# Optimization experiments

Measured on AMD Instinct MI355X. Metric: run time of the kernel, lower is better.

Reference implementation:

```python
import jax, jax.numpy as jnp
import numpy as np

NUM_LAYERS = 2
NUM_RES_LAYERS = 1  # residual add applied to layers i >= NUM_LAYERS - NUM_RES_LAYERS


def _lstm_seq(x, W, U, b, reverse):
    """Keras-style LSTM over full sequence. x:[B,T,E], W:[E,4H], U:[H,4H], b:[4H].
    Gate order i,f,g,o (Keras). reverse=True emulates go_backwards + K.reverse
    (lax.scan reverse=True keeps outputs time-aligned). Returns [B,T,H]."""
    B = x.shape[0]
    H = U.shape[0]
    # precompute input projections for all timesteps in one big matmul
    zx = jnp.einsum('bte,eg->btg', x, W) + b  # [B,T,4H]
    zx = jnp.swapaxes(zx, 0, 1)  # [T,B,4H]

    def step(carry, zxt):
        h, c = carry
        z = zxt + h @ U  # [B,4H]
        i, f, g, o = jnp.split(z, 4, axis=-1)
        i = jax.nn.sigmoid(i)
        f = jax.nn.sigmoid(f)
        g = jnp.tanh(g)
        o = jax.nn.sigmoid(o)
        c = f * c + i * g
        h = o * jnp.tanh(c)
        return (h, c), h

    init = (jnp.zeros((B, H), x.dtype), jnp.zeros((B, H), x.dtype))
    _, hs = jax.lax.scan(step, init, zx, reverse=reverse)  # [T,B,H]
    return jnp.swapaxes(hs, 0, 1)


def setup_inputs() -> dict:
    key = jax.random.key(0)
    k1, k2, k3 = jax.random.split(key, 3)
    B, T, E, H = 512, 200, 128, 128
    s = 0.05  # keep gates in a sane regime
    x = jax.random.normal(k1, (B, T, E), dtype=jnp.float32)
    W = jax.random.normal(k2, (NUM_LAYERS, 2, E, 4 * H), dtype=jnp.float32) * s
    U = jax.random.normal(k3, (NUM_LAYERS, 2, H, 4 * H), dtype=jnp.float32) * s
    b = jnp.ones((NUM_LAYERS, 2, 4 * H), dtype=jnp.float32)  # bias_initializer='ones'
    return {"x": x, "W": W, "U": U, "b": b}


def reference(x, W, U, b):
    # inference mode: dropout inactive
    input_fw = x
    input_bw = x
    for i in range(NUM_LAYERS):
        out_fw = _lstm_seq(input_fw, W[i, 0], U[i, 0], b[i, 0], reverse=False)
        out_bw = _lstm_seq(input_bw, W[i, 1], U[i, 1], b[i, 1], reverse=True)
        if i >= NUM_LAYERS - NUM_RES_LAYERS:
            out_fw = out_fw + input_fw
            out_bw = out_bw + input_bw
        input_fw = out_fw
        input_bw = out_bw
    # mode == 'ave'
    return (input_fw + input_bw) / 2
```

## Files before the change

kernel.cpp:

```cpp
#include <hip/hip_runtime.h>


typedef _Float16 f16;
typedef _Float16 f16x2 __attribute__((ext_vector_type(2)));
typedef _Float16 f16x4 __attribute__((ext_vector_type(4)));
typedef _Float16 f16x8 __attribute__((ext_vector_type(8)));
typedef float    f32x4 __attribute__((ext_vector_type(4)));

#define B_   512
#define T_   200
#define E_   128
#define H_   128
#define G4_  512
#define M_   (B_*T_)

static __device__ __forceinline__ float rcpa(float x) {
#if __has_builtin(__builtin_amdgcn_rcpf)
  return __builtin_amdgcn_rcpf(x);
#else
  return 1.f / x;
#endif
}
static __device__ __forceinline__ float exp2a(float x) {
#if __has_builtin(__builtin_amdgcn_exp2f)
  return __builtin_amdgcn_exp2f(x);
#else
  return exp2f(x);
#endif
}
static __device__ __forceinline__ f16x2 pk2(float lo, float hi) {
  return __builtin_bit_cast(f16x2, __builtin_amdgcn_cvt_pkrtz(lo, hi));
}

static __device__ __forceinline__ void lgkm_barrier() {
  asm volatile("s_waitcnt lgkmcnt(0)" ::: "memory");
  __builtin_amdgcn_s_barrier();
}

__global__ __launch_bounds__(256)
void cvt_x(const float* __restrict__ x, f16* __restrict__ xh) {
  const int n8 = M_ * E_ / 8;
  for (int i = blockIdx.x * 256 + threadIdx.x; i < n8; i += gridDim.x * 256) {
    const float4 a = ((const float4*)x)[i * 2];
    const float4 b = ((const float4*)x)[i * 2 + 1];
    f16x8 v;
    v[0] = (f16)a.x; v[1] = (f16)a.y; v[2] = (f16)a.z; v[3] = (f16)a.w;
    v[4] = (f16)b.x; v[5] = (f16)b.y; v[6] = (f16)b.z; v[7] = (f16)b.w;
    *(f16x8*)(xh + (size_t)i * 8) = v;
  }
}

__global__ __launch_bounds__(256)
void prep_w(const float* __restrict__ W, const float* __restrict__ U,
            f16* __restrict__ Wt, f16* __restrict__ Ut) {
  const int m = blockIdx.x;
  const float* s = (m < 4 ? W + (size_t)m * E_ * G4_ : U + (size_t)(m - 4) * E_ * G4_);
  f16* d        = (m < 4 ? Wt + (size_t)m * E_ * G4_ : Ut + (size_t)(m - 4) * E_ * G4_);
  for (int i = threadIdx.x; i < E_ * G4_; i += 256) {
    const int k = i >> 9, g = i & 511;
    float v = s[i];
    if ((g >> 7) == 2) v *= 2.f;
    d[(size_t)g * E_ + k] = (f16)v;
  }
}

template <int LAYER>
__global__ __launch_bounds__(512, 2)
void scan_fused(const f16* __restrict__ in,
                const f16* __restrict__ Utl,
                const f16* __restrict__ Wtl,
                const float* __restrict__ bl,
                const f16* __restrict__ res,
                f16* __restrict__ hout)
{
  __shared__ f16 hsh[2][16][136];

  const int tid  = threadIdx.x;
  const int lane = tid & 63;
  const int wv   = tid >> 6;
  const int row  = lane & 15;
  const int kg   = lane >> 4;
  const int bx   = blockIdx.x;
  const int dir  = bx >> 5;
  const int R0   = (bx & 31) * 16;
  const int coff = wv * 16 + kg * 4;

  const f16* Ud = Utl + (size_t)dir * G4_ * E_;
  const f16* Wd = Wtl + (size_t)dir * G4_ * E_;
  const float* bd = bl + (size_t)dir * G4_;
  const f16* ind  = in + (LAYER == 1 ? (size_t)dir * M_ * H_ : 0);
  f16* houtd      = hout + (size_t)dir * M_ * H_;

  f16x8 aU[4][4], aW[4][4];
#pragma unroll
  for (int g = 0; g < 4; ++g) {
    const size_t gcol = (size_t)(g * 128 + wv * 16 + row) * E_;
#pragma unroll
    for (int kk = 0; kk < 4; ++kk) {
      aU[g][kk] = *(const f16x8*)(Ud + gcol + kk * 32 + kg * 8);
      aW[g][kk] = *(const f16x8*)(Wd + gcol + kk * 32 + kg * 8);
    }
  }
  f32x4 zb[4];
#pragma unroll
  for (int g = 0; g < 4; ++g) {
#pragma unroll
    for (int i = 0; i < 4; ++i) {
      const float v = bd[g * 128 + coff + i];
      zb[g][i] = (g == 2) ? 2.f * v : v;
    }
  }

  for (int i = tid; i < 2 * 16 * 136; i += 512) ((f16*)hsh)[i] = (f16)0.f;

  const int t0 = dir ? (T_ - 1) : 0;
  const int ts = dir ? -1 : 1;

  const f16* inrow  = ind + (size_t)(R0 + row) * T_ * E_ + kg * 8;
  const f16* resrow = (LAYER == 1)
      ? res + (size_t)dir * M_ * H_ + (size_t)(R0 + row) * T_ * H_ + coff : nullptr;
  f16* outptr = houtd + (size_t)(R0 + row) * T_ * H_ + (size_t)t0 * H_ + coff;

  float cc0 = 0.f, cc1 = 0.f, cc2 = 0.f, cc3 = 0.f;

  const f16* xptrA = inrow + (long)(t0 + ts) * E_;
  const f16* xptrB = inrow + (long)(t0 + 2 * ts) * E_;
  f16x8 xpA[4], xpB[4], xP[4];
#pragma unroll
  for (int kk = 0; kk < 4; ++kk) {
    xP[kk]  = *(const f16x8*)(inrow + (long)t0 * E_ + kk * 32);
    xpA[kk] = *(const f16x8*)(xptrA + kk * 32);
    xpB[kk] = *(const f16x8*)(xptrB + kk * 32);
  }
  const f16* rptrA = nullptr; const f16* rptrB = nullptr;
  uint2 rvA = {}, rvB = {};
  if (LAYER == 1) {
    rptrA = resrow + (long)t0 * H_;
    rptrB = resrow + (long)(t0 + ts) * H_;
    rvA = *(const uint2*)rptrA;
    rvB = *(const uint2*)rptrB;
  }

  lgkm_barrier();

  f32x4 zA[4], zB[4];
#pragma unroll
  for (int g = 0; g < 4; ++g) {
    zA[g] = __builtin_amdgcn_mfma_f32_16x16x32_f16(aW[g][0], xP[0], zb[g], 0, 0, 0);
#pragma unroll
    for (int kk = 1; kk < 4; ++kk)
      zA[g] = __builtin_amdgcn_mfma_f32_16x16x32_f16(aW[g][kk], xP[kk], zA[g], 0, 0, 0);
  }

  constexpr float NL2E  = -1.4426950408889634f;
  constexpr float NL2E2 = -2.8853900817779268f;

  auto step = [&](f32x4 (&zc)[4], f32x4 (&zn)[4], f16x8 (&xp)[4],
                  const f16*& xptr, uint2& rv, const f16*& rptr,
                  int rp, int wp) {
    f16x8 hf[4];
#pragma unroll
    for (int kk = 0; kk < 4; ++kk) hf[kk] = *(const f16x8*)&hsh[rp][row][kk * 32 + kg * 8];

#pragma unroll
    for (int g = 0; g < 4; ++g)
      zn[g] = __builtin_amdgcn_mfma_f32_16x16x32_f16(aW[g][0], xp[0], zb[g], 0, 0, 0);
#pragma unroll
    for (int kk = 1; kk < 4; ++kk) {
      zn[0] = __builtin_amdgcn_mfma_f32_16x16x32_f16(aW[0][kk], xp[kk], zn[0], 0, 0, 0);
      zn[1] = __builtin_amdgcn_mfma_f32_16x16x32_f16(aW[1][kk], xp[kk], zn[1], 0, 0, 0);
      zn[2] = __builtin_amdgcn_mfma_f32_16x16x32_f16(aW[2][kk], xp[kk], zn[2], 0, 0, 0);
      zn[3] = __builtin_amdgcn_mfma_f32_16x16x32_f16(aW[3][kk], xp[kk], zn[3], 0, 0, 0);
    }

    xptr += 2 * ts * E_;
#pragma unroll
    for (int kk = 0; kk < 4; ++kk) xp[kk] = *(const f16x8*)(xptr + kk * 32);
    f16x2 rva, rvb;
    if (LAYER == 1) {
      rva = __builtin_bit_cast(f16x2, rv.x);
      rvb = __builtin_bit_cast(f16x2, rv.y);
      rptr += 2 * ts * H_;
      rv = *(const uint2*)rptr;
    }

#pragma unroll
    for (int kk = 0; kk < 4; ++kk) {
      zc[0] = __builtin_amdgcn_mfma_f32_16x16x32_f16(aU[0][kk], hf[kk], zc[0], 0, 0, 0);
      zc[1] = __builtin_amdgcn_mfma_f32_16x16x32_f16(aU[1][kk], hf[kk], zc[1], 0, 0, 0);
      zc[2] = __builtin_amdgcn_mfma_f32_16x16x32_f16(aU[2][kk], hf[kk], zc[2], 0, 0, 0);
      zc[3] = __builtin_amdgcn_mfma_f32_16x16x32_f16(aU[3][kk], hf[kk], zc[3], 0, 0, 0);
    }

    float hv[4];
    float cc[4] = {cc0, cc1, cc2, cc3};
#pragma unroll
    for (int i = 0; i < 4; ++i) {
      const float ei = exp2a(zc[0][i] * NL2E);
      const float ef = exp2a(zc[1][i] * NL2E);
      const float eg = exp2a(zc[2][i] * NL2E);
      const float eo = exp2a(zc[3][i] * NL2E);
      const float ig = rcpa(1.f + ei);
      const float fg = rcpa(1.f + ef);
      const float gg = fmaf(2.f, rcpa(1.f + eg), -1.f);
      const float og = rcpa(1.f + eo);
      cc[i] = fmaf(fg, cc[i], ig * gg);
      const float ec = exp2a(cc[i] * NL2E2);
      const float tc = fmaf(2.f, rcpa(1.f + ec), -1.f);
      hv[i] = og * tc;
    }
    cc0 = cc[0]; cc1 = cc[1]; cc2 = cc[2]; cc3 = cc[3];

    const f16x2 h01 = pk2(hv[0], hv[1]);
    const f16x2 h23 = pk2(hv[2], hv[3]);
    uint2 hp;
    hp.x = __builtin_bit_cast(unsigned int, h01);
    hp.y = __builtin_bit_cast(unsigned int, h23);
    *(uint2*)&hsh[wp][row][coff] = hp;

    if (LAYER == 0) {
      *(uint2*)outptr = hp;
    } else {
      const f16x2 half2 = {(f16)0.5f, (f16)0.5f};
      const f16x2 o01 = (h01 + rva) * half2;
      const f16x2 o23 = (h23 + rvb) * half2;
      uint2 o;
      o.x = __builtin_bit_cast(unsigned int, o01);
      o.y = __builtin_bit_cast(unsigned int, o23);
      *(uint2*)outptr = o;
    }
    outptr += ts * H_;

    lgkm_barrier();
  };

  for (int k = 0; k < T_ / 2; ++k) {
    step(zA, zB, xpA, xptrA, rvA, rptrA, 0, 1);
    step(zB, zA, xpB, xptrB, rvB, rptrB, 1, 0);
  }
}

__global__ __launch_bounds__(256)
void final_add(const f16* __restrict__ a, const f16* __restrict__ b,
               float* __restrict__ o)
{
  const int n8 = M_ * H_ / 8;
  for (int i = blockIdx.x * 256 + threadIdx.x; i < n8; i += gridDim.x * 256) {
    const f16x8 va = *(const f16x8*)(a + (size_t)i * 8);
    const f16x8 vb = *(const f16x8*)(b + (size_t)i * 8);
    float4 o0, o1;
    o0.x = (float)va[0] + (float)vb[0];  o0.y = (float)va[1] + (float)vb[1];
    o0.z = (float)va[2] + (float)vb[2];  o0.w = (float)va[3] + (float)vb[3];
    o1.x = (float)va[4] + (float)vb[4];  o1.y = (float)va[5] + (float)vb[5];
    o1.z = (float)va[6] + (float)vb[6];  o1.w = (float)va[7] + (float)vb[7];
    *(float4*)(o + (size_t)i * 8)     = o0;
    *(float4*)(o + (size_t)i * 8 + 4) = o1;
  }
}

extern "C" void kernel_launch(void* const* d_in, const int* in_sizes, int n_in,
                              void* d_out, int out_size, void* d_ws, size_t ws_size,
                              hipStream_t stream) {
  const float* x = (const float*)d_in[0];
  const float* W = (const float*)d_in[1];
  const float* U = (const float*)d_in[2];
  const float* b = (const float*)d_in[3];
  float* out = (float*)d_out;

  char* ws = (char*)d_ws;
  f16* xh = (f16*)(ws + 2048);
  f16* h0 = xh + (size_t)M_ * E_ + 1024;
  f16* h1 = h0 + (size_t)2 * M_ * H_ + 1024;
  f16* Wt = h1 + (size_t)2 * M_ * H_ + 1024;
  f16* Ut = Wt + (size_t)4 * G4_ * E_;

  const size_t WTL = (size_t)2 * G4_ * E_;
  const size_t BL  = 2 * G4_;

  cvt_x<<<dim3(2048), 256, 0, stream>>>(x, xh);
  prep_w<<<dim3(8), 256, 0, stream>>>(W, U, Wt, Ut);
  scan_fused<0><<<dim3(64), 512, 0, stream>>>(xh, Ut, Wt, b, nullptr, h0);
  scan_fused<1><<<dim3(64), 512, 0, stream>>>(h0, Ut + WTL, Wt + WTL, b + BL, h0, h1);
  final_add<<<dim3(2048), 256, 0, stream>>>(h1, h1 + (size_t)M_ * H_, out);
}
```

Baseline: 636.1 us.

## Interleave input-projection MFMAs with gate math and fold log2e into weights

The -log2(e) scale factor is folded into the W and U weights and into the bias at prep time, which removes the per-gate multiply before exp2. The next step's input-projection MFMAs are spread through the gate-activation loop so matrix work overlaps the transcendental ALU work. The barrier now sits right after the shared-memory h write, and the global output store plus the next x and residual loads come after it, so they overlap the next step. Scaling the weights before the f16 conversion slightly changes rounding.

Measured after the change: 728.7 us. 14.5% more time.

```diff
diff --git a/kernel.cpp b/kernel.cpp
--- a/kernel.cpp
+++ b/kernel.cpp
@@ -56,11 +56,11 @@
   const int m = blockIdx.x;
   const float* s = (m < 4 ? W + (size_t)m * E_ * G4_ : U + (size_t)(m - 4) * E_ * G4_);
   f16* d        = (m < 4 ? Wt + (size_t)m * E_ * G4_ : Ut + (size_t)(m - 4) * E_ * G4_);
+  const float L2E = 1.4426950408889634f;
   for (int i = threadIdx.x; i < E_ * G4_; i += 256) {
     const int k = i >> 9, g = i & 511;
-    float v = s[i];
-    if ((g >> 7) == 2) v *= 2.f;
-    d[(size_t)g * E_ + k] = (f16)v;
+    const float sc = ((g >> 7) == 2) ? -2.f * L2E : -L2E;
+    d[(size_t)g * E_ + k] = (f16)(s[i] * sc);
   }
 }
 
@@ -101,13 +101,14 @@
       aW[g][kk] = *(const f16x8*)(Wd + gcol + kk * 32 + kg * 8);
     }
   }
+  const float L2E = 1.4426950408889634f;
   f32x4 zb[4];
 #pragma unroll
   for (int g = 0; g < 4; ++g) {
 #pragma unroll
     for (int i = 0; i < 4; ++i) {
       const float v = bd[g * 128 + coff + i];
-      zb[g][i] = (g == 2) ? 2.f * v : v;
+      zb[g][i] = v * ((g == 2) ? -2.f * L2E : -L2E);
     }
   }
 
@@ -152,7 +153,6 @@
       zA[g] = __builtin_amdgcn_mfma_f32_16x16x32_f16(aW[g][kk], xP[kk], zA[g], 0, 0, 0);
   }
 
-  constexpr float NL2E  = -1.4426950408889634f;
   constexpr float NL2E2 = -2.8853900817779268f;
 
   auto step = [&](f32x4 (&zc)[4], f32x4 (&zn)[4], f16x8 (&xp)[4],
@@ -161,28 +161,6 @@
     f16x8 hf[4];
 #pragma unroll
     for (int kk = 0; kk < 4; ++kk) hf[kk] = *(const f16x8*)&hsh[rp][row][kk * 32 + kg * 8];
-
-#pragma unroll
-    for (int g = 0; g < 4; ++g)
-      zn[g] = __builtin_amdgcn_mfma_f32_16x16x32_f16(aW[g][0], xp[0], zb[g], 0, 0, 0);
-#pragma unroll
-    for (int kk = 1; kk < 4; ++kk) {
-      zn[0] = __builtin_amdgcn_mfma_f32_16x16x32_f16(aW[0][kk], xp[kk], zn[0], 0, 0, 0);
-      zn[1] = __builtin_amdgcn_mfma_f32_16x16x32_f16(aW[1][kk], xp[kk], zn[1], 0, 0, 0);
-      zn[2] = __builtin_amdgcn_mfma_f32_16x16x32_f16(aW[2][kk], xp[kk], zn[2], 0, 0, 0);
-      zn[3] = __builtin_amdgcn_mfma_f32_16x16x32_f16(aW[3][kk], xp[kk], zn[3], 0, 0, 0);
-    }
-
-    xptr += 2 * ts * E_;
-#pragma unroll
-    for (int kk = 0; kk < 4; ++kk) xp[kk] = *(const f16x8*)(xptr + kk * 32);
-    f16x2 rva, rvb;
-    if (LAYER == 1) {
-      rva = __builtin_bit_cast(f16x2, rv.x);
-      rvb = __builtin_bit_cast(f16x2, rv.y);
-      rptr += 2 * ts * H_;
-      rv = *(const uint2*)rptr;
-    }
 
 #pragma unroll
     for (int kk = 0; kk < 4; ++kk) {
@@ -196,10 +174,21 @@
     float cc[4] = {cc0, cc1, cc2, cc3};
 #pragma unroll
     for (int i = 0; i < 4; ++i) {
-      const float ei = exp2a(zc[0][i] * NL2E);
-      const float ef = exp2a(zc[1][i] * NL2E);
-      const float eg = exp2a(zc[2][i] * NL2E);
-      const float eo = exp2a(zc[3][i] * NL2E);
+      if (i == 0) {
+        zn[0] = __builtin_amdgcn_mfma_f32_16x16x32_f16(aW[0][0], xp[0], zb[0], 0, 0, 0);
+        zn[1] = __builtin_amdgcn_mfma_f32_16x16x32_f16(aW[1][0], xp[0], zb[1], 0, 0, 0);
+        zn[2] = __builtin_amdgcn_mfma_f32_16x16x32_f16(aW[2][0], xp[0], zb[2], 0, 0, 0);
+        zn[3] = __builtin_amdgcn_mfma_f32_16x16x32_f16(aW[3][0], xp[0], zb[3], 0, 0, 0);
+      } else {
+        zn[0] = __builtin_amdgcn_mfma_f32_16x16x32_f16(aW[0][i], xp[i], zn[0], 0, 0, 0);
+        zn[1] = __builtin_amdgcn_mfma_f32_16x16x32_f16(aW[1][i], xp[i], zn[1], 0, 0, 0);
+        zn[2] = __builtin_amdgcn_mfma_f32_16x16x32_f16(aW[2][i], xp[i], zn[2], 0, 0, 0);
+        zn[3] = __builtin_amdgcn_mfma_f32_16x16x32_f16(aW[3][i], xp[i], zn[3], 0, 0, 0);
+      }
+      const float ei = exp2a(zc[0][i]);
+      const float ef = exp2a(zc[1][i]);
+      const float eg = exp2a(zc[2][i]);
+      const float eo = exp2a(zc[3][i]);
       const float ig = rcpa(1.f + ei);
       const float fg = rcpa(1.f + ef);
       const float gg = fmaf(2.f, rcpa(1.f + eg), -1.f);
@@ -218,20 +207,27 @@
     hp.y = __builtin_bit_cast(unsigned int, h23);
     *(uint2*)&hsh[wp][row][coff] = hp;
 
+    lgkm_barrier();
+
     if (LAYER == 0) {
       *(uint2*)outptr = hp;
     } else {
       const f16x2 half2 = {(f16)0.5f, (f16)0.5f};
+      const f16x2 rva = __builtin_bit_cast(f16x2, rv.x);
+      const f16x2 rvb = __builtin_bit_cast(f16x2, rv.y);
       const f16x2 o01 = (h01 + rva) * half2;
       const f16x2 o23 = (h23 + rvb) * half2;
       uint2 o;
       o.x = __builtin_bit_cast(unsigned int, o01);
       o.y = __builtin_bit_cast(unsigned int, o23);
       *(uint2*)outptr = o;
+      rptr += 2 * ts * H_;
+      rv = *(const uint2*)rptr;
     }
     outptr += ts * H_;
-
-    lgkm_barrier();
+    xptr += 2 * ts * E_;
+#pragma unroll
+    for (int kk = 0; kk < 4; ++kk) xp[kk] = *(const f16x8*)(xptr + kk * 32);
   };
 
   for (int k = 0; k < T_ / 2; ++k) {
```

## Hoist input projection out of LSTM scan into a separate parallel GEMM

Applied to the files above, without the earlier changes.

The input-projection matmul (x·W + b) for every timestep now runs in a standalone tiled MFMA GEMM over the whole grid, for both directions. The result is stored as an f16 z buffer, with the -log2(e) and gate-specific scale already folded into W and b. The recurrent scan kernel then only does the h·U MFMAs and the gate math each step, prefetching the precomputed z two steps ahead. U is loaded from fp32 and transposed through shared memory inside the scan, which drops the separate weight and x conversion kernels. The aim is to shorten the per-step serial critical path on only 64 blocks. The cost is writing and re-reading a large z intermediate in memory, plus extra precision loss from storing pre-activations in f16.

Measured after the change: 795.0 us. 1.25x slower.

```diff
diff --git a/kernel.cpp b/kernel.cpp
--- a/kernel.cpp
+++ b/kernel.cpp
@@ -14,6 +14,9 @@
 #define G4_  512
 #define M_   (B_*T_)
 
+constexpr float NL2E  = -1.4426950408889634f;
+constexpr float NL2E2 = -2.8853900817779268f;
+
 static __device__ __forceinline__ float rcpa(float x) {
 #if __has_builtin(__builtin_amdgcn_rcpf)
   return __builtin_amdgcn_rcpf(x);
@@ -31,48 +34,105 @@
 static __device__ __forceinline__ f16x2 pk2(float lo, float hi) {
   return __builtin_bit_cast(f16x2, __builtin_amdgcn_cvt_pkrtz(lo, hi));
 }
-
 static __device__ __forceinline__ void lgkm_barrier() {
   asm volatile("s_waitcnt lgkmcnt(0)" ::: "memory");
   __builtin_amdgcn_s_barrier();
 }
 
+template <typename AT>
 __global__ __launch_bounds__(256)
-void cvt_x(const float* __restrict__ x, f16* __restrict__ xh) {
-  const int n8 = M_ * E_ / 8;
-  for (int i = blockIdx.x * 256 + threadIdx.x; i < n8; i += gridDim.x * 256) {
-    const float4 a = ((const float4*)x)[i * 2];
-    const float4 b = ((const float4*)x)[i * 2 + 1];
-    f16x8 v;
-    v[0] = (f16)a.x; v[1] = (f16)a.y; v[2] = (f16)a.z; v[3] = (f16)a.w;
-    v[4] = (f16)b.x; v[5] = (f16)b.y; v[6] = (f16)b.z; v[7] = (f16)b.w;
-    *(f16x8*)(xh + (size_t)i * 8) = v;
-  }
-}
-
-__global__ __launch_bounds__(256)
-void prep_w(const float* __restrict__ W, const float* __restrict__ U,
-            f16* __restrict__ Wt, f16* __restrict__ Ut) {
-  const int m = blockIdx.x;
-  const float* s = (m < 4 ? W + (size_t)m * E_ * G4_ : U + (size_t)(m - 4) * E_ * G4_);
-  f16* d        = (m < 4 ? Wt + (size_t)m * E_ * G4_ : Ut + (size_t)(m - 4) * E_ * G4_);
-  for (int i = threadIdx.x; i < E_ * G4_; i += 256) {
-    const int k = i >> 9, g = i & 511;
-    float v = s[i];
-    if ((g >> 7) == 2) v *= 2.f;
-    d[(size_t)g * E_ + k] = (f16)v;
+void gemm_zx(const AT* __restrict__ A0, const AT* __restrict__ A1,
+             const float* __restrict__ Wl,
+             const float* __restrict__ bl,
+             f16* __restrict__ zx)
+{
+  __shared__ f16 Ash[128 * 136];
+  __shared__ f16 Bsh[64 * 136];
+
+  const int n0  = blockIdx.x * 64;
+  const int m0  = blockIdx.y * 128;
+  const int dir = blockIdx.z;
+  const AT* A = dir ? A1 : A0;
+  const float* Wd = Wl + (size_t)dir * E_ * G4_;
+  const float* bd = bl + (size_t)dir * G4_;
+  const int tid = threadIdx.x;
+
+#pragma unroll
+  for (int it = 0; it < 16; ++it) {
+    int idx = tid + it * 256;
+    int row = idx >> 5, c4 = idx & 31;
+    if constexpr (sizeof(AT) == 4) {
+      const float4 v = *(const float4*)(A + (size_t)(m0 + row) * E_ + c4 * 4);
+      f16x2 p0; p0[0] = (f16)v.x; p0[1] = (f16)v.y;
+      f16x2 p1; p1[0] = (f16)v.z; p1[1] = (f16)v.w;
+      uint2 w2; w2.x = __builtin_bit_cast(unsigned int, p0); w2.y = __builtin_bit_cast(unsigned int, p1);
+      *(uint2*)&Ash[row * 136 + c4 * 4] = w2;
+    } else {
+      const uint2 v = *(const uint2*)(A + (size_t)(m0 + row) * E_ + c4 * 4);
+      *(uint2*)&Ash[row * 136 + c4 * 4] = v;
+    }
+  }
+#pragma unroll
+  for (int it = 0; it < 8; ++it) {
+    int idx = tid + it * 256;
+    int k = idx >> 4, n4 = idx & 15;
+    const int g = n0 + n4 * 4;
+    const float sc = ((g >> 7) == 2) ? NL2E2 : NL2E;
+    const float4 v = *(const float4*)(Wd + (size_t)k * G4_ + g);
+    Bsh[(n4 * 4 + 0) * 136 + k] = (f16)(v.x * sc);
+    Bsh[(n4 * 4 + 1) * 136 + k] = (f16)(v.y * sc);
+    Bsh[(n4 * 4 + 2) * 136 + k] = (f16)(v.z * sc);
+    Bsh[(n4 * 4 + 3) * 136 + k] = (f16)(v.w * sc);
+  }
+  __syncthreads();
+
+  const int w = tid >> 6, l = tid & 63;
+  const int lr = l & 15, lk = (l >> 4) * 8;
+  f32x4 acc[2][4] = {};
+
+#pragma unroll
+  for (int kc = 0; kc < 4; ++kc) {
+    const int kb = kc * 32 + lk;
+    f16x8 a0 = *(const f16x8*)&Ash[(w * 32 + 0  + lr) * 136 + kb];
+    f16x8 a1 = *(const f16x8*)&Ash[(w * 32 + 16 + lr) * 136 + kb];
+    f16x8 b0 = *(const f16x8*)&Bsh[(0  + lr) * 136 + kb];
+    f16x8 b1 = *(const f16x8*)&Bsh[(16 + lr) * 136 + kb];
+    f16x8 b2 = *(const f16x8*)&Bsh[(32 + lr) * 136 + kb];
+    f16x8 b3 = *(const f16x8*)&Bsh[(48 + lr) * 136 + kb];
+    acc[0][0] = __builtin_amdgcn_mfma_f32_16x16x32_f16(a0, b0, acc[0][0], 0, 0, 0);
+    acc[0][1] = __builtin_amdgcn_mfma_f32_16x16x32_f16(a0, b1, acc[0][1], 0, 0, 0);
+    acc[0][2] = __builtin_amdgcn_mfma_f32_16x16x32_f16(a0, b2, acc[0][2], 0, 0, 0);
+    acc[0][3] = __builtin_amdgcn_mfma_f32_16x16x32_f16(a0, b3, acc[0][3], 0, 0, 0);
+    acc[1][0] = __builtin_amdgcn_mfma_f32_16x16x32_f16(a1, b0, acc[1][0], 0, 0, 0);
+    acc[1][1] = __builtin_amdgcn_mfma_f32_16x16x32_f16(a1, b1, acc[1][1], 0, 0, 0);
+    acc[1][2] = __builtin_amdgcn_mfma_f32_16x16x32_f16(a1, b2, acc[1][2], 0, 0, 0);
+    acc[1][3] = __builtin_amdgcn_mfma_f32_16x16x32_f16(a1, b3, acc[1][3], 0, 0, 0);
+  }
+
+#pragma unroll
+  for (int mf = 0; mf < 2; ++mf) {
+#pragma unroll
+    for (int nf = 0; nf < 4; ++nf) {
+      const int g = n0 + nf * 16 + lr;
+      const float sc = ((g >> 7) == 2) ? NL2E2 : NL2E;
+      const float bias = bd[g] * sc;
+#pragma unroll
+      for (int i = 0; i < 4; ++i) {
+        const int m = m0 + w * 32 + mf * 16 + (l >> 4) * 4 + i;
+        zx[((size_t)dir * M_ + m) * G4_ + g] = (f16)(acc[mf][nf][i] + bias);
+      }
+    }
   }
 }
 
 template <int LAYER>
 __global__ __launch_bounds__(512, 2)
-void scan_fused(const f16* __restrict__ in,
-                const f16* __restrict__ Utl,
-                const f16* __restrict__ Wtl,
-                const float* __restrict__ bl,
-                const f16* __restrict__ res,
-                f16* __restrict__ hout)
+void scan_u(const f16* __restrict__ zx,
+            const float* __restrict__ Ul,
+            const f16* __restrict__ res,
+            f16* __restrict__ hout)
 {
+  __shared__ f16 Ush[32][520];
   __shared__ f16 hsh[2][16][136];
 
   const int tid  = threadIdx.x;
@@ -85,30 +145,35 @@
   const int R0   = (bx & 31) * 16;
   const int coff = wv * 16 + kg * 4;
 
-  const f16* Ud = Utl + (size_t)dir * G4_ * E_;
-  const f16* Wd = Wtl + (size_t)dir * G4_ * E_;
-  const float* bd = bl + (size_t)dir * G4_;
-  const f16* ind  = in + (LAYER == 1 ? (size_t)dir * M_ * H_ : 0);
-  f16* houtd      = hout + (size_t)dir * M_ * H_;
-
-  f16x8 aU[4][4], aW[4][4];
-#pragma unroll
-  for (int g = 0; g < 4; ++g) {
-    const size_t gcol = (size_t)(g * 128 + wv * 16 + row) * E_;
-#pragma unroll
-    for (int kk = 0; kk < 4; ++kk) {
-      aU[g][kk] = *(const f16x8*)(Ud + gcol + kk * 32 + kg * 8);
-      aW[g][kk] = *(const f16x8*)(Wd + gcol + kk * 32 + kg * 8);
-    }
-  }
-  f32x4 zb[4];
-#pragma unroll
-  for (int g = 0; g < 4; ++g) {
-#pragma unroll
-    for (int i = 0; i < 4; ++i) {
-      const float v = bd[g * 128 + coff + i];
-      zb[g][i] = (g == 2) ? 2.f * v : v;
-    }
+  const float* Udr = Ul + (size_t)dir * H_ * G4_;
+  const f16* zxd   = zx + (size_t)dir * M_ * G4_;
+  f16* houtd       = hout + (size_t)dir * M_ * H_;
+
+  f16x8 aU[4][4];
+#pragma unroll
+  for (int c = 0; c < 4; ++c) {
+#pragma unroll
+    for (int it = 0; it < 8; ++it) {
+      const int idx = tid + it * 512;
+      const int kl = idx >> 7, g4 = idx & 127;
+      const float4 v = *(const float4*)(Udr + (size_t)(c * 32 + kl) * G4_ + g4 * 4);
+      const int g = g4 * 4;
+      const float sc = ((g >> 7) == 2) ? NL2E2 : NL2E;
+      Ush[kl][g + 0] = (f16)(v.x * sc);
+      Ush[kl][g + 1] = (f16)(v.y * sc);
+      Ush[kl][g + 2] = (f16)(v.z * sc);
+      Ush[kl][g + 3] = (f16)(v.w * sc);
+    }
+    __syncthreads();
+#pragma unroll
+    for (int g = 0; g < 4; ++g) {
+      const int gcol = g * 128 + wv * 16 + row;
+      f16x8 t;
+#pragma unroll
+      for (int j = 0; j < 8; ++j) t[j] = Ush[kg * 8 + j][gcol];
+      aU[g][c] = t;
+    }
+    __syncthreads();
   }
 
   for (int i = tid; i < 2 * 16 * 136; i += 512) ((f16*)hsh)[i] = (f16)0.f;
@@ -116,90 +181,72 @@
   const int t0 = dir ? (T_ - 1) : 0;
   const int ts = dir ? -1 : 1;
 
-  const f16* inrow  = ind + (size_t)(R0 + row) * T_ * E_ + kg * 8;
-  const f16* resrow = (LAYER == 1)
-      ? res + (size_t)dir * M_ * H_ + (size_t)(R0 + row) * T_ * H_ + coff : nullptr;
-  f16* outptr = houtd + (size_t)(R0 + row) * T_ * H_ + (size_t)t0 * H_ + coff;
-
-  float cc0 = 0.f, cc1 = 0.f, cc2 = 0.f, cc3 = 0.f;
-
-  const f16* xptrA = inrow + (long)(t0 + ts) * E_;
-  const f16* xptrB = inrow + (long)(t0 + 2 * ts) * E_;
-  f16x8 xpA[4], xpB[4], xP[4];
-#pragma unroll
-  for (int kk = 0; kk < 4; ++kk) {
-    xP[kk]  = *(const f16x8*)(inrow + (long)t0 * E_ + kk * 32);
-    xpA[kk] = *(const f16x8*)(xptrA + kk * 32);
-    xpB[kk] = *(const f16x8*)(xptrB + kk * 32);
+  const f16* zrow = zxd + ((size_t)(R0 + row) * T_ + t0) * G4_ + coff;
+  const f16* zptrA = zrow;
+  const f16* zptrB = zrow + (long)ts * G4_;
+  f16x4 zpA[4], zpB[4];
+#pragma unroll
+  for (int g = 0; g < 4; ++g) {
+    zpA[g] = *(const f16x4*)(zptrA + g * 128);
+    zpB[g] = *(const f16x4*)(zptrB + g * 128);
   }
   const f16* rptrA = nullptr; const f16* rptrB = nullptr;
   uint2 rvA = {}, rvB = {};
   if (LAYER == 1) {
+    const f16* resrow = res + (size_t)dir * M_ * H_ + (size_t)(R0 + row) * T_ * H_ + coff;
     rptrA = resrow + (long)t0 * H_;
     rptrB = resrow + (long)(t0 + ts) * H_;
     rvA = *(const uint2*)rptrA;
     rvB = *(const uint2*)rptrB;
   }
+  f16* outptr = houtd + (size_t)(R0 + row) * T_ * H_ + (size_t)t0 * H_ + coff;
+
+  float cc0 = 0.f, cc1 = 0.f, cc2 = 0.f, cc3 = 0.f;
 
   lgkm_barrier();
 
-  f32x4 zA[4], zB[4];
-#pragma unroll
-  for (int g = 0; g < 4; ++g) {
-    zA[g] = __builtin_amdgcn_mfma_f32_16x16x32_f16(aW[g][0], xP[0], zb[g], 0, 0, 0);
-#pragma unroll
-    for (int kk = 1; kk < 4; ++kk)
-      zA[g] = __builtin_amdgcn_mfma_f32_16x16x32_f16(aW[g][kk], xP[kk], zA[g], 0, 0, 0);
-  }
-
-  constexpr float NL2E  = -1.4426950408889634f;
-  constexpr float NL2E2 = -2.8853900817779268f;
-
-  auto step = [&](f32x4 (&zc)[4], f32x4 (&zn)[4], f16x8 (&xp)[4],
-                  const f16*& xptr, uint2& rv, const f16*& rptr,
+  auto step = [&](f16x4 (&zp)[4], const f16*& zptr, uint2& rv, const f16*& rptr,
                   int rp, int wp) {
     f16x8 hf[4];
 #pragma unroll
     for (int kk = 0; kk < 4; ++kk) hf[kk] = *(const f16x8*)&hsh[rp][row][kk * 32 + kg * 8];
 
-#pragma unroll
-    for (int g = 0; g < 4; ++g)
-      zn[g] = __builtin_amdgcn_mfma_f32_16x16x32_f16(aW[g][0], xp[0], zb[g], 0, 0, 0);
-#pragma unroll
-    for (int kk = 1; kk < 4; ++kk) {
-      zn[0] = __builtin_amdgcn_mfma_f32_16x16x32_f16(aW[0][kk], xp[kk], zn[0], 0, 0, 0);
-      zn[1] = __builtin_amdgcn_mfma_f32_16x16x32_f16(aW[1][kk], xp[kk], zn[1], 0, 0, 0);
-      zn[2] = __builtin_amdgcn_mfma_f32_16x16x32_f16(aW[2][kk], xp[kk], zn[2], 0, 0, 0);
-      zn[3] = __builtin_amdgcn_mfma_f32_16x16x32_f16(aW[3][kk], xp[kk], zn[3], 0, 0, 0);
-    }
-
-    xptr += 2 * ts * E_;
-#pragma unroll
-    for (int kk = 0; kk < 4; ++kk) xp[kk] = *(const f16x8*)(xptr + kk * 32);
+    f32x4 z[4];
+#pragma unroll
+    for (int g = 0; g < 4; ++g) {
+#pragma unroll
+      for (int i = 0; i < 4; ++i) z[g][i] = (float)zp[g][i];
+    }
     f16x2 rva, rvb;
     if (LAYER == 1) {
       rva = __builtin_bit_cast(f16x2, rv.x);
       rvb = __builtin_bit_cast(f16x2, rv.y);
+    }
+
+    zptr += 2 * ts * G4_;
+#pragma unroll
+    for (int g = 0; g < 4; ++g) zp[g] = *(const f16x4*)(zptr + g * 128);
+    if (LAYER == 1) {
       rptr += 2 * ts * H_;
       rv = *(const uint2*)rptr;
     }
 
 #pragma unroll
     for (int kk = 0; kk < 4; ++kk) {
-      zc[0] = __builtin_amdgcn_mfma_f32_16x16x32_f16(aU[0][kk], hf[kk], zc[0], 0, 0, 0);
-      zc[1] = __builtin_amdgcn_mfma_f32_16x16x32_f16(aU[1][kk], hf[kk], zc[1], 0, 0, 0);
-      zc[2] = __builtin_amdgcn_mfma_f32_16x16x32_f16(aU[2][kk], hf[kk], zc[2], 0, 0, 0);
-      zc[3] = __builtin_amdgcn_mfma_f32_16x16x32_f16(aU[3][kk], hf[kk], zc[3], 0, 0, 0);
+      z[0] = __builtin_amdgcn_mfma_f32_16x16x32_f16(aU[0][kk], hf[kk], z[0], 0, 0, 0);
+      z[1] = __builtin_amdgcn_mfma_f32_16x16x32_f16(aU[1][kk], hf[kk], z[1], 0, 0, 0);
+      z[2] = __builtin_amdgcn_mfma_f32_16x16x32_f16(aU[2][kk], hf[kk], z[2], 0, 0, 0);
+      z[3] = __builtin_amdgcn_mfma_f32_16x16x32_f16(aU[3][kk], hf[kk], z[3], 0, 0, 0);
     }
 
     float hv[4];
     float cc[4] = {cc0, cc1, cc2, cc3};
 #pragma unroll
     for (int i = 0; i < 4; ++i) {
-      const float ei = exp2a(zc[0][i] * NL2E);
-      const float ef = exp2a(zc[1][i] * NL2E);
-      const float eg = exp2a(zc[2][i] * NL2E);
-      const float eo = exp2a(zc[3][i] * NL2E);
+      const float ei = exp2a(z[0][i]);
+      const float ef = exp2a(z[1][i]);
+      const float eg = exp2a(z[2][i]);
+      const float eo = exp2a(z[3][i]);
       const float ig = rcpa(1.f + ei);
       const float fg = rcpa(1.f + ef);
       const float gg = fmaf(2.f, rcpa(1.f + eg), -1.f);
@@ -235,8 +282,8 @@
   };
 
   for (int k = 0; k < T_ / 2; ++k) {
-    step(zA, zB, xpA, xptrA, rvA, rptrA, 0, 1);
-    step(zB, zA, xpB, xptrB, rvB, rptrB, 1, 0);
+    step(zpA, zptrA, rvA, rptrA, 0, 1);
+    step(zpB, zptrB, rvB, rptrB, 1, 0);
   }
 }
 
@@ -268,18 +315,16 @@
   float* out = (float*)d_out;
 
   char* ws = (char*)d_ws;
-  f16* xh = (f16*)(ws + 2048);
-  f16* h0 = xh + (size_t)M_ * E_ + 1024;
-  f16* h1 = h0 + (size_t)2 * M_ * H_ + 1024;
-  f16* Wt = h1 + (size_t)2 * M_ * H_ + 1024;
-  f16* Ut = Wt + (size_t)4 * G4_ * E_;
-
-  const size_t WTL = (size_t)2 * G4_ * E_;
-  const size_t BL  = 2 * G4_;
-
-  cvt_x<<<dim3(2048), 256, 0, stream>>>(x, xh);
-  prep_w<<<dim3(8), 256, 0, stream>>>(W, U, Wt, Ut);
-  scan_fused<0><<<dim3(64), 512, 0, stream>>>(xh, Ut, Wt, b, nullptr, h0);
-  scan_fused<1><<<dim3(64), 512, 0, stream>>>(h0, Ut + WTL, Wt + WTL, b + BL, h0, h1);
-  final_add<<<dim3(2048), 256, 0, stream>>>(h1, h1 + (size_t)M_ * H_, out);
-}
+  f16* zx = (f16*)ws;
+  f16* h0 = (f16*)(ws + (size_t)2 * M_ * G4_ * 2);
+
+  const size_t WL = (size_t)2 * E_ * G4_;
+  const size_t BL = 2 * G4_;
+
+  dim3 gg(G4_ / 64, M_ / 128, 2);
+  gemm_zx<float><<<gg, 256, 0, stream>>>(x, x, W, b, zx);
+  scan_u<0><<<dim3(64), 512, 0, stream>>>(zx, U, nullptr, h0);
+  gemm_zx<f16><<<gg, 256, 0, stream>>>(h0, h0 + (size_t)M_ * H_, W + WL, b + BL, zx);
+  scan_u<1><<<dim3(64), 512, 0, stream>>>(zx, U + WL, h0, h0);
+  final_add<<<dim3(2048), 256, 0, stream>>>(h0, h0 + (size_t)M_ * H_, out);
+}
```

## Halve waves per scan block, give each wave two column tiles, fold log2e scale into weights

Applied to the files above, without the earlier changes.

The recurrent scan kernel now runs 4 waves of 256 threads instead of 8. Each wave computes two 16-column tiles, so it holds twice the W/U fragments in registers. This cuts barrier participants and the per-step synchronisation cost, but puts more serial MFMA work on each wave and raises register pressure. The -log2(e) and -2·log2(e) gate scaling is folded into the f16 weights and bias in prep, removing per-element multiplies, at some f16 precision risk. The cross-step software pipelining of the input projection is also dropped, so x-projection MFMAs are now issued in the same step as the recurrent ones.

Result: slower. 709.3 us (+11.5%).

```diff
diff --git a/kernel.cpp b/kernel.cpp
--- a/kernel.cpp
+++ b/kernel.cpp
@@ -14,6 +14,9 @@
 #define G4_  512
 #define M_   (B_*T_)
 
+constexpr float NL2E  = -1.4426950408889634f;
+constexpr float NL2E2 = -2.8853900817779268f;
+
 static __device__ __forceinline__ float rcpa(float x) {
 #if __has_builtin(__builtin_amdgcn_rcpf)
   return __builtin_amdgcn_rcpf(x);
@@ -31,7 +34,6 @@
 static __device__ __forceinline__ f16x2 pk2(float lo, float hi) {
   return __builtin_bit_cast(f16x2, __builtin_amdgcn_cvt_pkrtz(lo, hi));
 }
-
 static __device__ __forceinline__ void lgkm_barrier() {
   asm volatile("s_waitcnt lgkmcnt(0)" ::: "memory");
   __builtin_amdgcn_s_barrier();
@@ -58,14 +60,13 @@
   f16* d        = (m < 4 ? Wt + (size_t)m * E_ * G4_ : Ut + (size_t)(m - 4) * E_ * G4_);
   for (int i = threadIdx.x; i < E_ * G4_; i += 256) {
     const int k = i >> 9, g = i & 511;
-    float v = s[i];
-    if ((g >> 7) == 2) v *= 2.f;
-    d[(size_t)g * E_ + k] = (f16)v;
+    const float sc = ((g >> 7) == 2) ? NL2E2 : NL2E;
+    d[(size_t)g * E_ + k] = (f16)(s[i] * sc);
   }
 }
 
 template <int LAYER>
-__global__ __launch_bounds__(512, 2)
+__global__ __launch_bounds__(256, 1)
 void scan_fused(const f16* __restrict__ in,
                 const f16* __restrict__ Utl,
                 const f16* __restrict__ Wtl,
@@ -83,7 +84,7 @@
   const int bx   = blockIdx.x;
   const int dir  = bx >> 5;
   const int R0   = (bx & 31) * 16;
-  const int coff = wv * 16 + kg * 4;
+  const int c0   = wv * 32 + kg * 4;
 
   const f16* Ud = Utl + (size_t)dir * G4_ * E_;
   const f16* Wd = Wtl + (size_t)dir * G4_ * E_;
@@ -91,143 +92,157 @@
   const f16* ind  = in + (LAYER == 1 ? (size_t)dir * M_ * H_ : 0);
   f16* houtd      = hout + (size_t)dir * M_ * H_;
 
-  f16x8 aU[4][4], aW[4][4];
+  f16x8 aU[4][2][4], aW[4][2][4];
 #pragma unroll
   for (int g = 0; g < 4; ++g) {
-    const size_t gcol = (size_t)(g * 128 + wv * 16 + row) * E_;
-#pragma unroll
-    for (int kk = 0; kk < 4; ++kk) {
-      aU[g][kk] = *(const f16x8*)(Ud + gcol + kk * 32 + kg * 8);
-      aW[g][kk] = *(const f16x8*)(Wd + gcol + kk * 32 + kg * 8);
-    }
-  }
-  f32x4 zb[4];
+#pragma unroll
+    for (int ct = 0; ct < 2; ++ct) {
+      const size_t gcol = (size_t)(g * 128 + wv * 32 + ct * 16 + row) * E_;
+#pragma unroll
+      for (int kk = 0; kk < 4; ++kk) {
+        aU[g][ct][kk] = *(const f16x8*)(Ud + gcol + kk * 32 + kg * 8);
+        aW[g][ct][kk] = *(const f16x8*)(Wd + gcol + kk * 32 + kg * 8);
+      }
+    }
+  }
+  f32x4 zb[4][2];
 #pragma unroll
   for (int g = 0; g < 4; ++g) {
 #pragma unroll
-    for (int i = 0; i < 4; ++i) {
-      const float v = bd[g * 128 + coff + i];
-      zb[g][i] = (g == 2) ? 2.f * v : v;
-    }
-  }
-
-  for (int i = tid; i < 2 * 16 * 136; i += 512) ((f16*)hsh)[i] = (f16)0.f;
+    for (int ct = 0; ct < 2; ++ct) {
+#pragma unroll
+      for (int i = 0; i < 4; ++i) {
+        const float v = bd[g * 128 + wv * 32 + ct * 16 + kg * 4 + i];
+        zb[g][ct][i] = v * ((g == 2) ? NL2E2 : NL2E);
+      }
+    }
+  }
+
+  for (int i = tid; i < 2 * 16 * 136; i += 256) ((f16*)hsh)[i] = (f16)0.f;
 
   const int t0 = dir ? (T_ - 1) : 0;
   const int ts = dir ? -1 : 1;
 
   const f16* inrow  = ind + (size_t)(R0 + row) * T_ * E_ + kg * 8;
   const f16* resrow = (LAYER == 1)
-      ? res + (size_t)dir * M_ * H_ + (size_t)(R0 + row) * T_ * H_ + coff : nullptr;
-  f16* outptr = houtd + (size_t)(R0 + row) * T_ * H_ + (size_t)t0 * H_ + coff;
-
-  float cc0 = 0.f, cc1 = 0.f, cc2 = 0.f, cc3 = 0.f;
-
-  const f16* xptrA = inrow + (long)(t0 + ts) * E_;
-  const f16* xptrB = inrow + (long)(t0 + 2 * ts) * E_;
-  f16x8 xpA[4], xpB[4], xP[4];
+      ? res + (size_t)dir * M_ * H_ + (size_t)(R0 + row) * T_ * H_ + c0 : nullptr;
+  f16* outptr = houtd + (size_t)(R0 + row) * T_ * H_ + (size_t)t0 * H_ + c0;
+
+  float cc[8] = {0.f, 0.f, 0.f, 0.f, 0.f, 0.f, 0.f, 0.f};
+
+  const f16* xptrA = inrow + (long)t0 * E_;
+  const f16* xptrB = inrow + (long)(t0 + ts) * E_;
+  f16x8 xpA[4], xpB[4];
 #pragma unroll
   for (int kk = 0; kk < 4; ++kk) {
-    xP[kk]  = *(const f16x8*)(inrow + (long)t0 * E_ + kk * 32);
     xpA[kk] = *(const f16x8*)(xptrA + kk * 32);
     xpB[kk] = *(const f16x8*)(xptrB + kk * 32);
   }
   const f16* rptrA = nullptr; const f16* rptrB = nullptr;
-  uint2 rvA = {}, rvB = {};
+  uint2 rvA[2] = {}, rvB[2] = {};
   if (LAYER == 1) {
     rptrA = resrow + (long)t0 * H_;
     rptrB = resrow + (long)(t0 + ts) * H_;
-    rvA = *(const uint2*)rptrA;
-    rvB = *(const uint2*)rptrB;
+    rvA[0] = *(const uint2*)rptrA;      rvA[1] = *(const uint2*)(rptrA + 16);
+    rvB[0] = *(const uint2*)rptrB;      rvB[1] = *(const uint2*)(rptrB + 16);
   }
 
   lgkm_barrier();
 
-  f32x4 zA[4], zB[4];
-#pragma unroll
-  for (int g = 0; g < 4; ++g) {
-    zA[g] = __builtin_amdgcn_mfma_f32_16x16x32_f16(aW[g][0], xP[0], zb[g], 0, 0, 0);
-#pragma unroll
-    for (int kk = 1; kk < 4; ++kk)
-      zA[g] = __builtin_amdgcn_mfma_f32_16x16x32_f16(aW[g][kk], xP[kk], zA[g], 0, 0, 0);
-  }
-
-  constexpr float NL2E  = -1.4426950408889634f;
-  constexpr float NL2E2 = -2.8853900817779268f;
-
-  auto step = [&](f32x4 (&zc)[4], f32x4 (&zn)[4], f16x8 (&xp)[4],
-                  const f16*& xptr, uint2& rv, const f16*& rptr,
-                  int rp, int wp) {
+  auto step = [&](f16x8 (&xp)[4], const f16*& xptr, uint2 (&rv)[2],
+                  const f16*& rptr, int rp, int wp) {
     f16x8 hf[4];
 #pragma unroll
     for (int kk = 0; kk < 4; ++kk) hf[kk] = *(const f16x8*)&hsh[rp][row][kk * 32 + kg * 8];
 
-#pragma unroll
-    for (int g = 0; g < 4; ++g)
-      zn[g] = __builtin_amdgcn_mfma_f32_16x16x32_f16(aW[g][0], xp[0], zb[g], 0, 0, 0);
+    f16x8 xf[4];
+#pragma unroll
+    for (int kk = 0; kk < 4; ++kk) xf[kk] = xp[kk];
+    f16x2 rva[2], rvb[2];
+    if (LAYER == 1) {
+#pragma unroll
+      for (int ct = 0; ct < 2; ++ct) {
+        rva[ct] = __builtin_bit_cast(f16x2, rv[ct].x);
+        rvb[ct] = __builtin_bit_cast(f16x2, rv[ct].y);
+      }
+    }
+
+    xptr += 2 * ts * E_;
+#pragma unroll
+    for (int kk = 0; kk < 4; ++kk) xp[kk] = *(const f16x8*)(xptr + kk * 32);
+    if (LAYER == 1) {
+      rptr += 2 * ts * H_;
+      rv[0] = *(const uint2*)rptr;
+      rv[1] = *(const uint2*)(rptr + 16);
+    }
+
+    f32x4 z[4][2];
+#pragma unroll
+    for (int g = 0; g < 4; ++g) {
+#pragma unroll
+      for (int ct = 0; ct < 2; ++ct)
+        z[g][ct] = __builtin_amdgcn_mfma_f32_16x16x32_f16(aW[g][ct][0], xf[0], zb[g][ct], 0, 0, 0);
+    }
 #pragma unroll
     for (int kk = 1; kk < 4; ++kk) {
-      zn[0] = __builtin_amdgcn_mfma_f32_16x16x32_f16(aW[0][kk], xp[kk], zn[0], 0, 0, 0);
-      zn[1] = __builtin_amdgcn_mfma_f32_16x16x32_f16(aW[1][kk], xp[kk], zn[1], 0, 0, 0);
-      zn[2] = __builtin_amdgcn_mfma_f32_16x16x32_f16(aW[2][kk], xp[kk], zn[2], 0, 0, 0);
-      zn[3] = __builtin_amdgcn_mfma_f32_16x16x32_f16(aW[3][kk], xp[kk], zn[3], 0, 0, 0);
-    }
-
-    xptr += 2 * ts * E_;
-#pragma unroll
-    for (int kk = 0; kk < 4; ++kk) xp[kk] = *(const f16x8*)(xptr + kk * 32);
-    f16x2 rva, rvb;
-    if (LAYER == 1) {
-      rva = __builtin_bit_cast(f16x2, rv.x);
-      rvb = __builtin_bit_cast(f16x2, rv.y);
-      rptr += 2 * ts * H_;
-      rv = *(const uint2*)rptr;
-    }
-
+#pragma unroll
+      for (int g = 0; g < 4; ++g) {
+#pragma unroll
+        for (int ct = 0; ct < 2; ++ct)
+          z[g][ct] = __builtin_amdgcn_mfma_f32_16x16x32_f16(aW[g][ct][kk], xf[kk], z[g][ct], 0, 0, 0);
+      }
+    }
 #pragma unroll
     for (int kk = 0; kk < 4; ++kk) {
-      zc[0] = __builtin_amdgcn_mfma_f32_16x16x32_f16(aU[0][kk], hf[kk], zc[0], 0, 0, 0);
-      zc[1] = __builtin_amdgcn_mfma_f32_16x16x32_f16(aU[1][kk], hf[kk], zc[1], 0, 0, 0);
-      zc[2] = __builtin_amdgcn_mfma_f32_16x16x32_f16(aU[2][kk], hf[kk], zc[2], 0, 0, 0);
-      zc[3] = __builtin_amdgcn_mfma_f32_16x16x32_f16(aU[3][kk], hf[kk], zc[3], 0, 0, 0);
-    }
-
-    float hv[4];
-    float cc[4] = {cc0, cc1, cc2, cc3};
-#pragma unroll
-    for (int i = 0; i < 4; ++i) {
-      const float ei = exp2a(zc[0][i] * NL2E);
-      const float ef = exp2a(zc[1][i] * NL2E);
-      const float eg = exp2a(zc[2][i] * NL2E);
-      const float eo = exp2a(zc[3][i] * NL2E);
-      const float ig = rcpa(1.f + ei);
-      const float fg = rcpa(1.f + ef);
-      const float gg = fmaf(2.f, rcpa(1.f + eg), -1.f);
-      const float og = rcpa(1.f + eo);
-      cc[i] = fmaf(fg, cc[i], ig * gg);
-      const float ec = exp2a(cc[i] * NL2E2);
-      const float tc = fmaf(2.f, rcpa(1.f + ec), -1.f);
-      hv[i] = og * tc;
-    }
-    cc0 = cc[0]; cc1 = cc[1]; cc2 = cc[2]; cc3 = cc[3];
-
-    const f16x2 h01 = pk2(hv[0], hv[1]);
-    const f16x2 h23 = pk2(hv[2], hv[3]);
-    uint2 hp;
-    hp.x = __builtin_bit_cast(unsigned int, h01);
-    hp.y = __builtin_bit_cast(unsigned int, h23);
-    *(uint2*)&hsh[wp][row][coff] = hp;
+#pragma unroll
+      for (int g = 0; g < 4; ++g) {
+#pragma unroll
+        for (int ct = 0; ct < 2; ++ct)
+          z[g][ct] = __builtin_amdgcn_mfma_f32_16x16x32_f16(aU[g][ct][kk], hf[kk], z[g][ct], 0, 0, 0);
+      }
+    }
+
+    float hv[8];
+#pragma unroll
+    for (int ct = 0; ct < 2; ++ct) {
+#pragma unroll
+      for (int i = 0; i < 4; ++i) {
+        const int c = ct * 4 + i;
+        const float ig = rcpa(1.f + exp2a(z[0][ct][i]));
+        const float fg = rcpa(1.f + exp2a(z[1][ct][i]));
+        const float gg = fmaf(2.f, rcpa(1.f + exp2a(z[2][ct][i])), -1.f);
+        const float og = rcpa(1.f + exp2a(z[3][ct][i]));
+        cc[c] = fmaf(fg, cc[c], ig * gg);
+        const float tc = fmaf(2.f, rcpa(1.f + exp2a(cc[c] * NL2E2)), -1.f);
+        hv[c] = og * tc;
+      }
+    }
+
+    uint2 hp[2];
+#pragma unroll
+    for (int ct = 0; ct < 2; ++ct) {
+      const f16x2 h01 = pk2(hv[ct * 4 + 0], hv[ct * 4 + 1]);
+      const f16x2 h23 = pk2(hv[ct * 4 + 2], hv[ct * 4 + 3]);
+      hp[ct].x = __builtin_bit_cast(unsigned int, h01);
+      hp[ct].y = __builtin_bit_cast(unsigned int, h23);
+    }
+    *(uint2*)&hsh[wp][row][c0]      = hp[0];
+    *(uint2*)&hsh[wp][row][c0 + 16] = hp[1];
 
     if (LAYER == 0) {
-      *(uint2*)outptr = hp;
+      *(uint2*)outptr        = hp[0];
+      *(uint2*)(outptr + 16) = hp[1];
     } else {
       const f16x2 half2 = {(f16)0.5f, (f16)0.5f};
-      const f16x2 o01 = (h01 + rva) * half2;
-      const f16x2 o23 = (h23 + rvb) * half2;
-      uint2 o;
-      o.x = __builtin_bit_cast(unsigned int, o01);
-      o.y = __builtin_bit_cast(unsigned int, o23);
-      *(uint2*)outptr = o;
+#pragma unroll
+      for (int ct = 0; ct < 2; ++ct) {
+        const f16x2 o01 = (__builtin_bit_cast(f16x2, hp[ct].x) + rva[ct]) * half2;
+        const f16x2 o23 = (__builtin_bit_cast(f16x2, hp[ct].y) + rvb[ct]) * half2;
+        uint2 o;
+        o.x = __builtin_bit_cast(unsigned int, o01);
+        o.y = __builtin_bit_cast(unsigned int, o23);
+        *(uint2*)(outptr + ct * 16) = o;
+      }
     }
     outptr += ts * H_;
 
@@ -235,8 +250,8 @@
   };
 
   for (int k = 0; k < T_ / 2; ++k) {
-    step(zA, zB, xpA, xptrA, rvA, rptrA, 0, 1);
-    step(zB, zA, xpB, xptrB, rvB, rptrB, 1, 0);
+    step(xpA, xptrA, rvA, rptrA, k == 0 ? 0 : 0, 1);
+    step(xpB, xptrB, rvB, rptrB, 1, 0);
   }
 }
 
@@ -279,7 +294,7 @@
 
   cvt_x<<<dim3(2048), 256, 0, stream>>>(x, xh);
   prep_w<<<dim3(8), 256, 0, stream>>>(W, U, Wt, Ut);
-  scan_fused<0><<<dim3(64), 512, 0, stream>>>(xh, Ut, Wt, b, nullptr, h0);
-  scan_fused<1><<<dim3(64), 512, 0, stream>>>(h0, Ut + WTL, Wt + WTL, b + BL, h0, h1);
+  scan_fused<0><<<dim3(64), 256, 0, stream>>>(xh, Ut, Wt, b, nullptr, h0);
+  scan_fused<1><<<dim3(64), 256, 0, stream>>>(h0, Ut + WTL, Wt + WTL, b + BL, h0, h1);
   final_add<<<dim3(2048), 256, 0, stream>>>(h1, h1 + (size_t)M_ * H_, out);
 }
```
